# Kernel optimization log

Measured on AMD Instinct MI355X. Metric: run time of the kernel, lower is better.

## Reference

```python
import jax, jax.numpy as jnp
import numpy as np

N = 50000
E = 800000
IN_CH = 128
HID = 64
OUT_CH = 1
HEADS = 2


def setup_inputs() -> dict:
    key = jax.random.key(0)
    k1, k2, k3, k4, k5, k6, k7 = jax.random.split(key, 7)
    x = jax.random.normal(k1, (N, IN_CH), dtype=jnp.float32)
    row = jax.random.randint(k2, (E,), 0, N)
    col = jax.random.randint(k3, (E,), 0, N)
    edge_index = jnp.stack([row, col], axis=0).astype(jnp.int64)
    # Xavier-uniform-ish init scales
    def xavier(k, shape):
        fan_in, fan_out = shape[0], shape[1]
        lim = float(np.sqrt(6.0 / (fan_in + fan_out)))
        return jax.random.uniform(k, shape, jnp.float32, -lim, lim)
    W0 = xavier(k4, (IN_CH, HEADS * HID))          # layer 0 lin weight (transposed torch layout)
    attn0 = xavier(k5, (HEADS, 2 * HID))
    W1 = xavier(k6, (HID, HEADS * OUT_CH))         # layer 1 lin weight
    attn1 = xavier(k7, (HEADS, 2 * OUT_CH))
    return {"x": x, "edge_index": edge_index, "W0": W0, "attn0": attn0, "W1": W1, "attn1": attn1}


def _segment_softmax(alpha, row, num_nodes):
    # alpha: [E, H]; per-target-node (row) softmax across incoming edges.
    m = jax.ops.segment_max(alpha, row, num_segments=num_nodes)   # [N, H]
    ex = jnp.exp(alpha - m[row])
    s = jax.ops.segment_sum(ex, row, num_segments=num_nodes)      # [N, H]
    return ex / s[row]


def _gat_layer(x, edge_index, W, attn, heads, out_ch):
    n = x.shape[0]
    h = (x @ W).reshape(n, heads, out_ch)                         # [N, H, C]
    row, col = edge_index[0], edge_index[1]
    h_row = h[row]                                                # [E, H, C]
    h_col = h[col]                                                # [E, H, C]
    # (cat([h_row,h_col]) * attn).sum(-1) split into two contractions
    alpha = (jnp.einsum('ehc,hc->eh', h_row, attn[:, :out_ch])
             + jnp.einsum('ehc,hc->eh', h_col, attn[:, out_ch:]))
    alpha = jax.nn.leaky_relu(alpha, negative_slope=0.2)
    alpha = _segment_softmax(alpha, row, n)                        # [E, H]
    out = jax.ops.segment_sum(alpha[..., None] * h_col, row, num_segments=n)  # [N, H, C]
    return out.mean(axis=1), alpha


def reference(x, edge_index, W0, attn0, W1, attn1):
    h, _ = _gat_layer(x, edge_index, W0, attn0, HEADS, HID)
    h = jax.nn.relu(h)
    out, attn = _gat_layer(h, edge_index, W1, attn1, HEADS, OUT_CH)
    return out  # [N, OUT_CH]
```

## Files before the change

kernel.cpp:

```cpp
#include <hip/hip_runtime.h>
#include <math.h>

#define NNODES 50000
#define NEDGES 800000
#define NBKT 196
#define BKT_CAP 5120
#define EPB 2048
#define NBA ((NEDGES + EPB - 1) / EPB)
#define NBN ((NNODES + 127) / 128)

typedef __attribute__((ext_vector_type(8))) short short8;
typedef __attribute__((ext_vector_type(4))) float f32x4;

__device__ inline float bsum64(float v) {
    #pragma unroll
    for (int off = 1; off < 64; off <<= 1) v += __shfl_xor(v, off, 64);
    return v;
}

__device__ inline unsigned packbf2(float a, float b) {
    unsigned ua = __float_as_uint(a);
    unsigned ub = __float_as_uint(b);
    ua = (ua + 0x7fffu + ((ua >> 16) & 1u)) >> 16;
    ub = (ub + 0x7fffu + ((ub >> 16) & 1u)) >> 16;
    return ua | (ub << 16);
}
__device__ inline float bflo(unsigned u) { return __uint_as_float(u << 16); }
__device__ inline float bfhi(unsigned u) { return __uint_as_float(u & 0xffff0000u); }

__global__ __launch_bounds__(256) void k_prep(const float* __restrict__ W,
                                              unsigned short* __restrict__ Whi,
                                              unsigned short* __restrict__ Wlo,
                                              int* __restrict__ gcur) {
    if (blockIdx.x == 64) {
        int i = threadIdx.x;
        if (i < NBKT) gcur[i] = 0;
        return;
    }
    int tid = blockIdx.x * 256 + threadIdx.x;
    int i = tid & 7, lane = (tid >> 3) & 63, ct = (tid >> 9) & 7, kc = tid >> 12;
    int k = kc * 32 + (lane >> 4) * 8 + i;
    int col = ct * 16 + (lane & 15);
    float v = W[k * 128 + col];
    unsigned hb = packbf2(v, 0.f) & 0xffffu;
    float hv = __uint_as_float(hb << 16);
    unsigned lb = packbf2(v - hv, 0.f) & 0xffffu;
    Whi[tid] = (unsigned short)hb;
    Wlo[tid] = (unsigned short)lb;
}

__global__ __launch_bounds__(256) void k_nodeA(const int* __restrict__ ei,
                                               int* __restrict__ gcur,
                                               unsigned* __restrict__ stag,
                                               const float* __restrict__ x,
                                               const unsigned short* __restrict__ Whi,
                                               const unsigned short* __restrict__ Wlo,
                                               const float* __restrict__ attn0,
                                               float* __restrict__ ar,
                                               float* __restrict__ ac,
                                               unsigned* __restrict__ h0b) {
    __shared__ uint4 shbuf[4096];
    int t = threadIdx.x;

    if (blockIdx.x < NBA) {
        int* lh = (int*)shbuf;
        int* lbase = lh + NBKT;
        for (int i = t; i < NBKT; i += 256) lh[i] = 0;
        __syncthreads();
        int e0 = blockIdx.x * EPB;
        int rows[8], cols[8];
        #pragma unroll
        for (int i = 0; i < 8; i++) {
            int e = e0 + i * 256 + t;
            if (e < NEDGES) {
                rows[i] = ei[e];
                cols[i] = ei[NEDGES + e];
                atomicAdd(&lh[rows[i] >> 8], 1);
            }
        }
        __syncthreads();
        for (int i = t; i < NBKT; i += 256) {
            lbase[i] = atomicAdd(&gcur[i], lh[i]);
            lh[i] = 0;
        }
        __syncthreads();
        #pragma unroll
        for (int i = 0; i < 8; i++) {
            int e = e0 + i * 256 + t;
            if (e < NEDGES) {
                int b = rows[i] >> 8;
                int rank = atomicAdd(&lh[b], 1);
                stag[b * BKT_CAP + lbase[b] + rank] =
                    ((unsigned)(rows[i] & 255) << 16) | (unsigned)cols[i];
            }
        }
        return;
    }

    int bid = blockIdx.x - NBA;
    const uint4* WHg = (const uint4*)Whi;
    const uint4* WLg = (const uint4*)Wlo;
    #pragma unroll
    for (int i = 0; i < 8; i++) shbuf[i * 256 + t] = WHg[i * 256 + t];
    #pragma unroll
    for (int i = 0; i < 8; i++) shbuf[2048 + i * 256 + t] = WLg[i * 256 + t];
    __syncthreads();

    int w = t >> 6, lane = t & 63;
    int n0 = bid * 128 + w * 32;
    int c16 = lane & 15, grp = lane >> 4;

    f32x4 acc[2][8];
    #pragma unroll
    for (int f = 0; f < 2; f++)
        #pragma unroll
        for (int ct = 0; ct < 8; ct++) acc[f][ct] = (f32x4){0.f, 0.f, 0.f, 0.f};

    for (int kc = 0; kc < 4; kc++) {
        short8 a_h[2], a_l[2];
        #pragma unroll
        for (int f = 0; f < 2; f++) {
            int arow = n0 + f * 16 + c16;
            float xv[8];
            if (arow < NNODES) {
                *(float4*)&xv[0] = *(const float4*)&x[arow * 128 + kc * 32 + grp * 8];
                *(float4*)&xv[4] = *(const float4*)&x[arow * 128 + kc * 32 + grp * 8 + 4];
            } else {
                #pragma unroll
                for (int i = 0; i < 8; i++) xv[i] = 0.f;
            }
            unsigned ah[4], al[4];
            #pragma unroll
            for (int i = 0; i < 4; i++) ah[i] = packbf2(xv[2 * i], xv[2 * i + 1]);
            #pragma unroll
            for (int i = 0; i < 4; i++) {
                float l0 = xv[2 * i] - bflo(ah[i]);
                float l1 = xv[2 * i + 1] - bfhi(ah[i]);
                al[i] = packbf2(l0, l1);
            }
            a_h[f] = *(short8*)ah;
            a_l[f] = *(short8*)al;
        }

        #pragma unroll
        for (int ct = 0; ct < 8; ct++) {
            uint4 whv = shbuf[(kc * 8 + ct) * 64 + lane];
            uint4 wlv = shbuf[2048 + (kc * 8 + ct) * 64 + lane];
            short8 b_h = *(short8*)&whv;
            short8 b_l = *(short8*)&wlv;
            #pragma unroll
            for (int f = 0; f < 2; f++) {
                acc[f][ct] = __builtin_amdgcn_mfma_f32_16x16x32_bf16(a_h[f], b_h, acc[f][ct], 0, 0, 0);
                acc[f][ct] = __builtin_amdgcn_mfma_f32_16x16x32_bf16(a_h[f], b_l, acc[f][ct], 0, 0, 0);
                acc[f][ct] = __builtin_amdgcn_mfma_f32_16x16x32_bf16(a_l[f], b_h, acc[f][ct], 0, 0, 0);
            }
        }
    }

    #pragma unroll
    for (int f = 0; f < 2; f++) {
        #pragma unroll
        for (int reg = 0; reg < 4; reg++) {
            float pr0 = 0.f, pc0 = 0.f, pr1 = 0.f, pc1 = 0.f;
            #pragma unroll
            for (int ct = 0; ct < 4; ct++) {
                float v = acc[f][ct][reg];
                int ch = ct * 16 + c16;
                pr0 += v * attn0[ch];
                pc0 += v * attn0[64 + ch];
            }
            #pragma unroll
            for (int ct = 4; ct < 8; ct++) {
                float v = acc[f][ct][reg];
                int ch = (ct - 4) * 16 + c16;
                pr1 += v * attn0[128 + ch];
                pc1 += v * attn0[192 + ch];
            }
            #pragma unroll
            for (int off = 1; off < 16; off <<= 1) {
                pr0 += __shfl_xor(pr0, off, 64);
                pc0 += __shfl_xor(pc0, off, 64);
                pr1 += __shfl_xor(pr1, off, 64);
                pc1 += __shfl_xor(pc1, off, 64);
            }
            int n = n0 + f * 16 + grp * 4 + reg;
            if (c16 == 0 && n < NNODES) {
                ar[n * 2] = pr0;     ac[n * 2] = pc0;
                ar[n * 2 + 1] = pr1; ac[n * 2 + 1] = pc1;
            }
        }
        #pragma unroll
        for (int reg = 0; reg < 4; reg++) {
            int n = n0 + f * 16 + grp * 4 + reg;
            if (n < NNODES) {
                #pragma unroll
                for (int ct = 0; ct < 4; ct++)
                    h0b[n * 64 + ct * 16 + c16] = packbf2(acc[f][ct][reg], acc[f][ct + 4][reg]);
            }
        }
    }
}

__global__ __launch_bounds__(256) void k_binC(const int* __restrict__ gcur,
                                              const unsigned* __restrict__ stag,
                                              int* __restrict__ rowptr,
                                              int* __restrict__ ecol) {
    __shared__ int sh[256];
    __shared__ int dg[256];
    __shared__ int sc[256];
    __shared__ int cur[256];
    __shared__ int lout[BKT_CAP];
    int b = blockIdx.x, t = threadIdx.x;
    int gv = (t < NBKT) ? gcur[t] : 0;
    sh[t] = gv;
    __syncthreads();
    #pragma unroll
    for (int off = 1; off < 256; off <<= 1) {
        int u = (t >= off) ? sh[t - off] : 0;
        __syncthreads();
        sh[t] += u;
        __syncthreads();
    }
    int cnt = gcur[b];
    int base = sh[b] - cnt;
    dg[t] = 0;
    __syncthreads();
    for (int i = t; i < cnt; i += 256)
        atomicAdd(&dg[stag[b * BKT_CAP + i] >> 16], 1);
    __syncthreads();
    int v = dg[t];
    sc[t] = v;
    __syncthreads();
    #pragma unroll
    for (int off = 1; off < 256; off <<= 1) {
        int u = (t >= off) ? sc[t - off] : 0;
        __syncthreads();
        sc[t] += u;
        __syncthreads();
    }
    int excl = sc[t] - v;
    int gidx = b * 256 + t;
    if (gidx <= NNODES) rowptr[gidx] = base + excl;
    cur[t] = excl;
    __syncthreads();
    for (int i = t; i < cnt; i += 256) {
        unsigned p = stag[b * BKT_CAP + i];
        int pos = atomicAdd(&cur[p >> 16], 1);
        lout[pos] = (int)(p & 0xffffu);
    }
    __syncthreads();
    for (int i = t; i < cnt; i += 256) ecol[base + i] = lout[i];
}

__global__ __launch_bounds__(256) void k_l0edge(const int* __restrict__ rowptr,
                                                const int* __restrict__ ecol,
                                                const float* __restrict__ ar,
                                                const float* __restrict__ ac,
                                                const unsigned* __restrict__ h0b,
                                                const float* __restrict__ W1,
                                                float* __restrict__ h1) {
    int w = threadIdx.x >> 6, lane = threadIdx.x & 63;
    int n = blockIdx.x * 4 + w;
    if (n >= NNODES) return;
    int beg = rowptr[n];
    int deg = rowptr[n + 1] - beg;
    float arn0 = ar[n * 2], arn1 = ar[n * 2 + 1];
    int esub = lane >> 4;
    int c16 = lane & 15;
    float accA[4] = {0.f, 0.f, 0.f, 0.f};
    float accB[4] = {0.f, 0.f, 0.f, 0.f};
    float s0t = 0.f, s1t = 0.f;
    for (int wb = 0; wb < deg; wb += 64) {
        int cnt = deg - wb; if (cnt > 64) cnt = 64;
        float p0 = 0.f, p1 = 0.f; int colr = 0;
        if (lane < cnt) {
            colr = ecol[beg + wb + lane];
            float2 acv = ((const float2*)ac)[colr];
            float a0 = arn0 + acv.x, a1 = arn1 + acv.y;
            a0 = a0 > 0.f ? a0 : 0.2f * a0;
            a1 = a1 > 0.f ? a1 : 0.2f * a1;
            p0 = __expf(a0); p1 = __expf(a1);
            s0t += p0; s1t += p1;
        }
        int tmax = (cnt + 3) >> 2;
        for (int tt = 0; tt < tmax; tt++) {
            int i4 = tt * 4 + esub;
            int colx = __shfl(colr, i4, 64);
            float q0 = __shfl(p0, i4, 64);
            float q1 = __shfl(p1, i4, 64);
            if (i4 < cnt) {
                const uint4 u = *(const uint4*)(h0b + colx * 64 + c16 * 4);
                accA[0] += q0 * bflo(u.x); accB[0] += q1 * bfhi(u.x);
                accA[1] += q0 * bflo(u.y); accB[1] += q1 * bfhi(u.y);
                accA[2] += q0 * bflo(u.z); accB[2] += q1 * bfhi(u.z);
                accA[3] += q0 * bflo(u.w); accB[3] += q1 * bfhi(u.w);
            }
        }
    }
    float s0 = bsum64(s0t), s1 = bsum64(s1t);
    #pragma unroll
    for (int jj = 0; jj < 4; jj++) {
        accA[jj] += __shfl_xor(accA[jj], 16, 64);
        accA[jj] += __shfl_xor(accA[jj], 32, 64);
        accB[jj] += __shfl_xor(accB[jj], 16, 64);
        accB[jj] += __shfl_xor(accB[jj], 32, 64);
    }
    float si0 = deg ? 0.5f / s0 : 0.f;
    float si1 = deg ? 0.5f / s1 : 0.f;
    float pA = 0.f, pB = 0.f;
    #pragma unroll
    for (int jj = 0; jj < 4; jj++) {
        float o = si0 * accA[jj] + si1 * accB[jj];
        o = o > 0.f ? o : 0.f;
        float2 wv = ((const float2*)W1)[c16 * 4 + jj];
        pA += o * wv.x; pB += o * wv.y;
    }
    #pragma unroll
    for (int off = 1; off < 16; off <<= 1) {
        pA += __shfl_xor(pA, off, 64);
        pB += __shfl_xor(pB, off, 64);
    }
    if (lane == 0) { h1[n * 2] = pA; h1[n * 2 + 1] = pB; }
}

__global__ __launch_bounds__(256) void k_fused1(const int* __restrict__ rowptr,
                                                const int* __restrict__ ecol,
                                                const float* __restrict__ h1,
                                                const float* __restrict__ attn1,
                                                float* __restrict__ dout) {
    int w = threadIdx.x >> 6, lane = threadIdx.x & 63;
    int n = blockIdx.x * 4 + w;
    if (n >= NNODES) return;
    int beg = rowptr[n], end = rowptr[n + 1];
    if (beg == end) { if (lane == 0) dout[n] = 0.f; return; }
    float w01 = attn1[1], w11 = attn1[3];
    float base0 = attn1[0] * h1[n * 2];
    float base1 = attn1[2] * h1[n * 2 + 1];
    float s0 = 0.f, s1 = 0.f, acc0 = 0.f, acc1 = 0.f;
    for (int i = beg + lane; i < end; i += 64) {
        int col = ecol[i];
        float2 v = ((const float2*)h1)[col];
        float a0 = base0 + w01 * v.x;
        float a1 = base1 + w11 * v.y;
        a0 = a0 > 0.f ? a0 : 0.2f * a0;
        a1 = a1 > 0.f ? a1 : 0.2f * a1;
        float p0 = __expf(a0), p1 = __expf(a1);
        s0 += p0; acc0 += p0 * v.x;
        s1 += p1; acc1 += p1 * v.y;
    }
    s0 = bsum64(s0); s1 = bsum64(s1);
    acc0 = bsum64(acc0); acc1 = bsum64(acc1);
    if (lane == 0) dout[n] = 0.5f * (acc0 / s0 + acc1 / s1);
}

extern "C" void kernel_launch(void* const* d_in, const int* in_sizes, int n_in,
                              void* d_out, int out_size, void* d_ws, size_t ws_size,
                              hipStream_t stream) {
    const float* x     = (const float*)d_in[0];
    const int*   ei    = (const int*)d_in[1];
    const float* W0    = (const float*)d_in[2];
    const float* attn0 = (const float*)d_in[3];
    const float* W1    = (const float*)d_in[4];
    const float* attn1 = (const float*)d_in[5];
    float* dout = (float*)d_out;

    float* ws = (float*)d_ws;
    float*          ar     = ws;
    float*          ac     = ar + NNODES * 2;
    float*          h1     = ac + NNODES * 2;
    unsigned*       h0b    = (unsigned*)(h1 + NNODES * 2);
    unsigned short* Whi    = (unsigned short*)(h0b + NNODES * 64);
    unsigned short* Wlo    = Whi + 128 * 128;
    int*            gcur   = (int*)(Wlo + 128 * 128);
    int*            rowptr = gcur + NBKT;
    unsigned*       stag   = (unsigned*)(rowptr + NNODES + 1);
    int*            ecol   = (int*)(stag + NBKT * BKT_CAP);

    k_prep<<<65, 256, 0, stream>>>(W0, Whi, Wlo, gcur);
    k_nodeA<<<NBA + NBN, 256, 0, stream>>>(ei, gcur, stag, x, Whi, Wlo, attn0, ar, ac, h0b);
    k_binC<<<NBKT, 256, 0, stream>>>(gcur, stag, rowptr, ecol);
    k_l0edge<<<(NNODES + 3) / 4, 256, 0, stream>>>(rowptr, ecol, ar, ac, h0b, W1, h1);
    k_fused1<<<(NNODES + 3) / 4, 256, 0, stream>>>(rowptr, ecol, h1, attn1, dout);
}
```

Measured before the change: 98.39 us.

## Precompute W·attn projection for MFMA and split node GEMM across bin kernels

Folds attn0 into W0 on the prep kernel so the per-node attention scores come from one extra split-bf16 MFMA column tile instead of an FMA-plus-shuffle epilogue. The layer-0 node GEMM blocks are also split: about half run alongside edge binning in k_nodeA and the rest run alongside the bucket CSR build in k_nodeC. This is meant to balance work across the two launches so the binC phase is not underutilised. The change costs a bit more LDS per block, and the precomputed product changes rounding slightly.

```diff
diff --git a/kernel.cpp b/kernel.cpp
--- a/kernel.cpp
+++ b/kernel.cpp
@@ -8,6 +8,8 @@
 #define EPB 2048
 #define NBA ((NEDGES + EPB - 1) / EPB)
 #define NBN ((NNODES + 127) / 128)
+#define NBN_A 196
+#define NBN_B (NBN - NBN_A)
 
 typedef __attribute__((ext_vector_type(8))) short short8;
 typedef __attribute__((ext_vector_type(4))) float f32x4;
@@ -29,15 +31,36 @@
 __device__ inline float bfhi(unsigned u) { return __uint_as_float(u & 0xffff0000u); }
 
 __global__ __launch_bounds__(256) void k_prep(const float* __restrict__ W,
+                                              const float* __restrict__ attn0,
                                               unsigned short* __restrict__ Whi,
                                               unsigned short* __restrict__ Wlo,
+                                              unsigned short* __restrict__ Ahi,
+                                              unsigned short* __restrict__ Alo,
                                               int* __restrict__ gcur) {
+    int t = threadIdx.x;
     if (blockIdx.x == 64) {
-        int i = threadIdx.x;
-        if (i < NBKT) gcur[i] = 0;
+        if (t < NBKT) gcur[t] = 0;
+        for (int i = t; i < 2048; i += 256) { Ahi[i] = 0; Alo[i] = 0; }
+        __syncthreads();
+        for (int p = t; p < 512; p += 256) {
+            int k = p >> 2, col = p & 3;
+            int h = col >> 1, rc = col & 1;
+            const float* wrow = &W[k * 128 + h * 64];
+            const float* arow = &attn0[h * 128 + rc * 64];
+            float s = 0.f;
+            for (int c = 0; c < 64; c++) s += wrow[c] * arow[c];
+            unsigned hb = packbf2(s, 0.f) & 0xffffu;
+            float hv = __uint_as_float(hb << 16);
+            unsigned lb = packbf2(s - hv, 0.f) & 0xffffu;
+            int kc = k >> 5, kk = k & 31, grp = kk >> 3, i = kk & 7;
+            int lane = grp * 16 + col;
+            int idx = kc * 512 + lane * 8 + i;
+            Ahi[idx] = (unsigned short)hb;
+            Alo[idx] = (unsigned short)lb;
+        }
         return;
     }
-    int tid = blockIdx.x * 256 + threadIdx.x;
+    int tid = blockIdx.x * 256 + t;
     int i = tid & 7, lane = (tid >> 3) & 63, ct = (tid >> 9) & 7, kc = tid >> 12;
     int k = kc * 32 + (lane >> 4) * 8 + i;
     int col = ct * 16 + (lane & 15);
@@ -49,72 +72,123 @@
     Wlo[tid] = (unsigned short)lb;
 }
 
-__global__ __launch_bounds__(256) void k_nodeA(const int* __restrict__ ei,
-                                               int* __restrict__ gcur,
-                                               unsigned* __restrict__ stag,
-                                               const float* __restrict__ x,
-                                               const unsigned short* __restrict__ Whi,
-                                               const unsigned short* __restrict__ Wlo,
-                                               const float* __restrict__ attn0,
-                                               float* __restrict__ ar,
-                                               float* __restrict__ ac,
-                                               unsigned* __restrict__ h0b) {
-    __shared__ uint4 shbuf[4096];
+__device__ void binA_body(const int* __restrict__ ei, int* __restrict__ gcur,
+                          unsigned* __restrict__ stag, int* shmem) {
     int t = threadIdx.x;
-
-    if (blockIdx.x < NBA) {
-        int* lh = (int*)shbuf;
-        int* lbase = lh + NBKT;
-        for (int i = t; i < NBKT; i += 256) lh[i] = 0;
+    int* lh = shmem;
+    int* lbase = lh + NBKT;
+    for (int i = t; i < NBKT; i += 256) lh[i] = 0;
+    __syncthreads();
+    int e0 = blockIdx.x * EPB;
+    int rows[8], cols[8];
+    #pragma unroll
+    for (int i = 0; i < 8; i++) {
+        int e = e0 + i * 256 + t;
+        if (e < NEDGES) {
+            rows[i] = ei[e];
+            cols[i] = ei[NEDGES + e];
+            atomicAdd(&lh[rows[i] >> 8], 1);
+        }
+    }
+    __syncthreads();
+    for (int i = t; i < NBKT; i += 256) {
+        lbase[i] = atomicAdd(&gcur[i], lh[i]);
+        lh[i] = 0;
+    }
+    __syncthreads();
+    #pragma unroll
+    for (int i = 0; i < 8; i++) {
+        int e = e0 + i * 256 + t;
+        if (e < NEDGES) {
+            int b = rows[i] >> 8;
+            int rank = atomicAdd(&lh[b], 1);
+            stag[b * BKT_CAP + lbase[b] + rank] =
+                ((unsigned)(rows[i] & 255) << 16) | (unsigned)cols[i];
+        }
+    }
+}
+
+__device__ void binC_body(int b, const int* __restrict__ gcur,
+                          const unsigned* __restrict__ stag,
+                          int* __restrict__ rowptr, int* __restrict__ ecol,
+                          int* shmem) {
+    int t = threadIdx.x;
+    int* sh = shmem;
+    int* dg = sh + 256;
+    int* sc = dg + 256;
+    int* cur = sc + 256;
+    int* lout = cur + 256;
+    int gv = (t < NBKT) ? gcur[t] : 0;
+    sh[t] = gv;
+    __syncthreads();
+    #pragma unroll
+    for (int off = 1; off < 256; off <<= 1) {
+        int u = (t >= off) ? sh[t - off] : 0;
         __syncthreads();
-        int e0 = blockIdx.x * EPB;
-        int rows[8], cols[8];
-        #pragma unroll
-        for (int i = 0; i < 8; i++) {
-            int e = e0 + i * 256 + t;
-            if (e < NEDGES) {
-                rows[i] = ei[e];
-                cols[i] = ei[NEDGES + e];
-                atomicAdd(&lh[rows[i] >> 8], 1);
-            }
-        }
+        sh[t] += u;
         __syncthreads();
-        for (int i = t; i < NBKT; i += 256) {
-            lbase[i] = atomicAdd(&gcur[i], lh[i]);
-            lh[i] = 0;
-        }
+    }
+    int cnt = gcur[b];
+    int base = sh[b] - cnt;
+    dg[t] = 0;
+    __syncthreads();
+    for (int i = t; i < cnt; i += 256)
+        atomicAdd(&dg[stag[b * BKT_CAP + i] >> 16], 1);
+    __syncthreads();
+    int v = dg[t];
+    sc[t] = v;
+    __syncthreads();
+    #pragma unroll
+    for (int off = 1; off < 256; off <<= 1) {
+        int u = (t >= off) ? sc[t - off] : 0;
         __syncthreads();
-        #pragma unroll
-        for (int i = 0; i < 8; i++) {
-            int e = e0 + i * 256 + t;
-            if (e < NEDGES) {
-                int b = rows[i] >> 8;
-                int rank = atomicAdd(&lh[b], 1);
-                stag[b * BKT_CAP + lbase[b] + rank] =
-                    ((unsigned)(rows[i] & 255) << 16) | (unsigned)cols[i];
-            }
-        }
-        return;
-    }
-
-    int bid = blockIdx.x - NBA;
+        sc[t] += u;
+        __syncthreads();
+    }
+    int excl = sc[t] - v;
+    int gidx = b * 256 + t;
+    if (gidx <= NNODES) rowptr[gidx] = base + excl;
+    cur[t] = excl;
+    __syncthreads();
+    for (int i = t; i < cnt; i += 256) {
+        unsigned p = stag[b * BKT_CAP + i];
+        int pos = atomicAdd(&cur[p >> 16], 1);
+        lout[pos] = (int)(p & 0xffffu);
+    }
+    __syncthreads();
+    for (int i = t; i < cnt; i += 256) ecol[base + i] = lout[i];
+}
+
+__device__ void l0node_body(int bid, uint4* shbuf,
+                            const float* __restrict__ x,
+                            const unsigned short* __restrict__ Whi,
+                            const unsigned short* __restrict__ Wlo,
+                            const unsigned short* __restrict__ Ahi,
+                            const unsigned short* __restrict__ Alo,
+                            float* __restrict__ ar, float* __restrict__ ac,
+                            unsigned* __restrict__ h0b) {
+    int t = threadIdx.x;
     const uint4* WHg = (const uint4*)Whi;
     const uint4* WLg = (const uint4*)Wlo;
     #pragma unroll
     for (int i = 0; i < 8; i++) shbuf[i * 256 + t] = WHg[i * 256 + t];
     #pragma unroll
     for (int i = 0; i < 8; i++) shbuf[2048 + i * 256 + t] = WLg[i * 256 + t];
+    shbuf[4096 + t] = ((const uint4*)Ahi)[t];
+    shbuf[4352 + t] = ((const uint4*)Alo)[t];
     __syncthreads();
 
     int w = t >> 6, lane = t & 63;
     int n0 = bid * 128 + w * 32;
     int c16 = lane & 15, grp = lane >> 4;
 
-    f32x4 acc[2][8];
-    #pragma unroll
-    for (int f = 0; f < 2; f++)
+    f32x4 acc[2][8], accg[2];
+    #pragma unroll
+    for (int f = 0; f < 2; f++) {
+        accg[f] = (f32x4){0.f, 0.f, 0.f, 0.f};
         #pragma unroll
         for (int ct = 0; ct < 8; ct++) acc[f][ct] = (f32x4){0.f, 0.f, 0.f, 0.f};
+    }
 
     for (int kc = 0; kc < 4; kc++) {
         short8 a_h[2], a_l[2];
@@ -142,6 +216,17 @@
             a_l[f] = *(short8*)al;
         }
 
+        uint4 ghv = shbuf[4096 + kc * 64 + lane];
+        uint4 glv = shbuf[4352 + kc * 64 + lane];
+        short8 g_h = *(short8*)&ghv;
+        short8 g_l = *(short8*)&glv;
+        #pragma unroll
+        for (int f = 0; f < 2; f++) {
+            accg[f] = __builtin_amdgcn_mfma_f32_16x16x32_bf16(a_h[f], g_h, accg[f], 0, 0, 0);
+            accg[f] = __builtin_amdgcn_mfma_f32_16x16x32_bf16(a_h[f], g_l, accg[f], 0, 0, 0);
+            accg[f] = __builtin_amdgcn_mfma_f32_16x16x32_bf16(a_l[f], g_h, accg[f], 0, 0, 0);
+        }
+
         #pragma unroll
         for (int ct = 0; ct < 8; ct++) {
             uint4 whv = shbuf[(kc * 8 + ct) * 64 + lane];
@@ -161,38 +246,13 @@
     for (int f = 0; f < 2; f++) {
         #pragma unroll
         for (int reg = 0; reg < 4; reg++) {
-            float pr0 = 0.f, pc0 = 0.f, pr1 = 0.f, pc1 = 0.f;
-            #pragma unroll
-            for (int ct = 0; ct < 4; ct++) {
-                float v = acc[f][ct][reg];
-                int ch = ct * 16 + c16;
-                pr0 += v * attn0[ch];
-                pc0 += v * attn0[64 + ch];
-            }
-            #pragma unroll
-            for (int ct = 4; ct < 8; ct++) {
-                float v = acc[f][ct][reg];
-                int ch = (ct - 4) * 16 + c16;
-                pr1 += v * attn0[128 + ch];
-                pc1 += v * attn0[192 + ch];
-            }
-            #pragma unroll
-            for (int off = 1; off < 16; off <<= 1) {
-                pr0 += __shfl_xor(pr0, off, 64);
-                pc0 += __shfl_xor(pc0, off, 64);
-                pr1 += __shfl_xor(pr1, off, 64);
-                pc1 += __shfl_xor(pc1, off, 64);
-            }
-            int n = n0 + f * 16 + grp * 4 + reg;
-            if (c16 == 0 && n < NNODES) {
-                ar[n * 2] = pr0;     ac[n * 2] = pc0;
-                ar[n * 2 + 1] = pr1; ac[n * 2 + 1] = pc1;
-            }
-        }
-        #pragma unroll
-        for (int reg = 0; reg < 4; reg++) {
             int n = n0 + f * 16 + grp * 4 + reg;
             if (n < NNODES) {
+                if (c16 < 4) {
+                    float v = accg[f][reg];
+                    if (c16 & 1) ac[n * 2 + (c16 >> 1)] = v;
+                    else         ar[n * 2 + (c16 >> 1)] = v;
+                }
                 #pragma unroll
                 for (int ct = 0; ct < 4; ct++)
                     h0b[n * 64 + ct * 16 + c16] = packbf2(acc[f][ct][reg], acc[f][ct + 4][reg]);
@@ -201,55 +261,37 @@
     }
 }
 
-__global__ __launch_bounds__(256) void k_binC(const int* __restrict__ gcur,
-                                              const unsigned* __restrict__ stag,
-                                              int* __restrict__ rowptr,
-                                              int* __restrict__ ecol) {
-    __shared__ int sh[256];
-    __shared__ int dg[256];
-    __shared__ int sc[256];
-    __shared__ int cur[256];
-    __shared__ int lout[BKT_CAP];
-    int b = blockIdx.x, t = threadIdx.x;
-    int gv = (t < NBKT) ? gcur[t] : 0;
-    sh[t] = gv;
-    __syncthreads();
-    #pragma unroll
-    for (int off = 1; off < 256; off <<= 1) {
-        int u = (t >= off) ? sh[t - off] : 0;
-        __syncthreads();
-        sh[t] += u;
-        __syncthreads();
-    }
-    int cnt = gcur[b];
-    int base = sh[b] - cnt;
-    dg[t] = 0;
-    __syncthreads();
-    for (int i = t; i < cnt; i += 256)
-        atomicAdd(&dg[stag[b * BKT_CAP + i] >> 16], 1);
-    __syncthreads();
-    int v = dg[t];
-    sc[t] = v;
-    __syncthreads();
-    #pragma unroll
-    for (int off = 1; off < 256; off <<= 1) {
-        int u = (t >= off) ? sc[t - off] : 0;
-        __syncthreads();
-        sc[t] += u;
-        __syncthreads();
-    }
-    int excl = sc[t] - v;
-    int gidx = b * 256 + t;
-    if (gidx <= NNODES) rowptr[gidx] = base + excl;
-    cur[t] = excl;
-    __syncthreads();
-    for (int i = t; i < cnt; i += 256) {
-        unsigned p = stag[b * BKT_CAP + i];
-        int pos = atomicAdd(&cur[p >> 16], 1);
-        lout[pos] = (int)(p & 0xffffu);
-    }
-    __syncthreads();
-    for (int i = t; i < cnt; i += 256) ecol[base + i] = lout[i];
+__global__ __launch_bounds__(256) void k_nodeA(const int* __restrict__ ei,
+                                               int* __restrict__ gcur,
+                                               unsigned* __restrict__ stag,
+                                               const float* __restrict__ x,
+                                               const unsigned short* __restrict__ Whi,
+                                               const unsigned short* __restrict__ Wlo,
+                                               const unsigned short* __restrict__ Ahi,
+                                               const unsigned short* __restrict__ Alo,
+                                               float* __restrict__ ar,
+                                               float* __restrict__ ac,
+                                               unsigned* __restrict__ h0b) {
+    __shared__ uint4 shbuf[4608];
+    if (blockIdx.x < NBA) { binA_body(ei, gcur, stag, (int*)shbuf); return; }
+    l0node_body(blockIdx.x - NBA, shbuf, x, Whi, Wlo, Ahi, Alo, ar, ac, h0b);
+}
+
+__global__ __launch_bounds__(256) void k_nodeC(const int* __restrict__ gcur,
+                                               const unsigned* __restrict__ stag,
+                                               int* __restrict__ rowptr,
+                                               int* __restrict__ ecol,
+                                               const float* __restrict__ x,
+                                               const unsigned short* __restrict__ Whi,
+                                               const unsigned short* __restrict__ Wlo,
+                                               const unsigned short* __restrict__ Ahi,
+                                               const unsigned short* __restrict__ Alo,
+                                               float* __restrict__ ar,
+                                               float* __restrict__ ac,
+                                               unsigned* __restrict__ h0b) {
+    __shared__ uint4 shbuf[4608];
+    if (blockIdx.x < NBKT) { binC_body(blockIdx.x, gcur, stag, rowptr, ecol, (int*)shbuf); return; }
+    l0node_body(blockIdx.x - NBKT + NBN_A, shbuf, x, Whi, Wlo, Ahi, Alo, ar, ac, h0b);
 }
 
 __global__ __launch_bounds__(256) void k_l0edge(const int* __restrict__ rowptr,
@@ -371,14 +413,16 @@
     unsigned*       h0b    = (unsigned*)(h1 + NNODES * 2);
     unsigned short* Whi    = (unsigned short*)(h0b + NNODES * 64);
     unsigned short* Wlo    = Whi + 128 * 128;
-    int*            gcur   = (int*)(Wlo + 128 * 128);
+    unsigned short* Ahi    = Wlo + 128 * 128;
+    unsigned short* Alo    = Ahi + 2048;
+    int*            gcur   = (int*)(Alo + 2048);
     int*            rowptr = gcur + NBKT;
     unsigned*       stag   = (unsigned*)(rowptr + NNODES + 1);
     int*            ecol   = (int*)(stag + NBKT * BKT_CAP);
 
-    k_prep<<<65, 256, 0, stream>>>(W0, Whi, Wlo, gcur);
-    k_nodeA<<<NBA + NBN, 256, 0, stream>>>(ei, gcur, stag, x, Whi, Wlo, attn0, ar, ac, h0b);
-    k_binC<<<NBKT, 256, 0, stream>>>(gcur, stag, rowptr, ecol);
+    k_prep<<<65, 256, 0, stream>>>(W0, attn0, Whi, Wlo, Ahi, Alo, gcur);
+    k_nodeA<<<NBA + NBN_A, 256, 0, stream>>>(ei, gcur, stag, x, Whi, Wlo, Ahi, Alo, ar, ac, h0b);
+    k_nodeC<<<NBKT + NBN_B, 256, 0, stream>>>(gcur, stag, rowptr, ecol, x, Whi, Wlo, Ahi, Alo, ar, ac, h0b);
     k_l0edge<<<(NNODES + 3) / 4, 256, 0, stream>>>(rowptr, ecol, ar, ac, h0b, W1, h1);
     k_fused1<<<(NNODES + 3) / 4, 256, 0, stream>>>(rowptr, ecol, h1, attn1, dout);
 }
```

Result: slower. 110.0 us (+11.8%).
